# Kernel tuning notes

Measured on AMD Instinct MI355X. Metric: run time of the kernel, lower is better.

## Reference

```python
import jax, jax.numpy as jnp
import numpy as np

N = 100000          # total nodes
E = 1600000         # total edges
B = 500             # graphs in batch
NODES_PER_GRAPH = N // B
D_X, D_XDA = 96, 32
IN = D_X + D_XDA    # 128
HID = 128
OUT = 128


def setup_inputs() -> dict:
    key = jax.random.key(0)
    ks = jax.random.split(key, 12)
    s = 0.05
    x = jax.random.normal(ks[0], (N, D_X), jnp.float32)
    x_da = jax.random.normal(ks[1], (N, D_XDA), jnp.float32)
    edge_index = jax.random.randint(ks[2], (2, E), 0, N, jnp.int32).astype(jnp.int64)
    batch = (jnp.arange(N, dtype=jnp.int64) // NODES_PER_GRAPH)
    rootindex = jnp.arange(B, dtype=jnp.int64) * NODES_PER_GRAPH
    return {
        'x': x, 'x_da': x_da, 'edge_index': edge_index,
        'batch': batch, 'rootindex': rootindex,
        'td_w1': jax.random.normal(ks[3], (IN, HID), jnp.float32) * s,
        'td_b1': jnp.zeros((HID,), jnp.float32),
        'td_w2': jax.random.normal(ks[4], (HID + IN, OUT), jnp.float32) * s,
        'td_b2': jnp.zeros((OUT,), jnp.float32),
        'bu_w1': jax.random.normal(ks[5], (IN, HID), jnp.float32) * s,
        'bu_b1': jnp.zeros((HID,), jnp.float32),
        'bu_w2': jax.random.normal(ks[6], (HID + IN, OUT), jnp.float32) * s,
        'bu_b2': jnp.zeros((OUT,), jnp.float32),
        'mlp_w1': jax.random.normal(ks[7], ((OUT + HID) * 2, 2 * HID), jnp.float32) * s,
        'mlp_b1': jnp.zeros((2 * HID,), jnp.float32),
        'mlp_w2': jax.random.normal(ks[8], (2 * HID, 2), jnp.float32) * s,
        'mlp_b2': jnp.zeros((2,), jnp.float32),
    }


def gcn_conv(h, src, dst, W, b):
    # PyG GCNConv: h' = D^{-1/2} (A + I) D^{-1/2} (h W) + b,
    # messages flow src -> dst, deg counts incoming edges + self loop.
    h = h @ W                                              # [N, out]
    deg = jax.ops.segment_sum(jnp.ones((src.shape[0],), h.dtype), dst,
                              num_segments=N) + 1.0        # self loop
    dinv = jax.lax.rsqrt(deg)                              # deg >= 1
    norm = dinv[src] * dinv[dst]                           # [E]
    agg = jax.ops.segment_sum(h[src] * norm[:, None], dst, num_segments=N)
    agg = agg + h * (dinv * dinv)[:, None]                 # self-loop term
    return agg + b


def branch(x0, src, dst, w1, b1, w2, b2, batch, rootindex):
    # x0: [N, IN] = cat(x, x_da)
    x1 = x0
    h = gcn_conv(x0, src, dst, w1, b1)                     # [N, HID]
    x2 = h
    root1 = x1[rootindex[batch]]                           # root-extend gather
    h = jax.nn.relu(jnp.concatenate([h, root1], axis=1))   # dropout off (eval)
    h = jax.nn.relu(gcn_conv(h, src, dst, w2, b2))         # [N, OUT]
    root2 = x2[rootindex[batch]]
    h = jnp.concatenate([h, root2], axis=1)                # [N, OUT+HID]
    # scatter_mean over graphs
    sums = jax.ops.segment_sum(h, batch, num_segments=B)
    cnt = jax.ops.segment_sum(jnp.ones((N,), h.dtype), batch, num_segments=B)
    return sums / cnt[:, None]                             # [B, OUT+HID]


def reference(x, x_da, edge_index, batch, rootindex,
              td_w1, td_b1, td_w2, td_b2,
              bu_w1, bu_b1, bu_w2, bu_b2,
              mlp_w1, mlp_b1, mlp_w2, mlp_b2):
    x0 = jnp.concatenate([x, x_da], axis=1)                # [N, IN]
    src, dst = edge_index[0], edge_index[1]
    td = branch(x0, src, dst, td_w1, td_b1, td_w2, td_b2, batch, rootindex)
    bu = branch(x0, dst, src, bu_w1, bu_b1, bu_w2, bu_b2, batch, rootindex)
    g = jnp.concatenate([bu, td], axis=1)                  # [B, 4*HID]
    h = jax.nn.relu(g @ mlp_w1 + mlp_b1)
    return h @ mlp_w2 + mlp_b2                             # [B, 2]
```

## Files before the change

### kernel.cpp

```cpp
#include <hip/hip_runtime.h>

#define NN 100000
#define NE 1600000
#define NB 500
#define NPG 200
#define BS 128
#define NBUK 782
#define SLAB 2560
#define EPB3 2048
#define NEB3 782
#define NBLK 1563

typedef unsigned short ushortT;
typedef __attribute__((ext_vector_type(8))) short bf16x8;
typedef __attribute__((ext_vector_type(4))) float f32x4;

#define MFMA16(a, b, c) __builtin_amdgcn_mfma_f32_16x16x32_bf16(a, b, c, 0, 0, 0)

__device__ inline ushortT f2bf(float f) {
    unsigned u = __float_as_uint(f);
    return (ushortT)((u + 0x7FFF + ((u >> 16) & 1)) >> 16);
}
__device__ inline float bf2f(ushortT u) { return __uint_as_float((unsigned)u << 16); }
__device__ inline float4 bf4_to_f4(ushort4 u) {
    return make_float4(bf2f(u.x), bf2f(u.y), bf2f(u.z), bf2f(u.w));
}
__device__ inline bf16x8 cvt8(float4 f0, float4 f1) {
    bf16x8 r;
    r[0] = (short)f2bf(f0.x); r[1] = (short)f2bf(f0.y);
    r[2] = (short)f2bf(f0.z); r[3] = (short)f2bf(f0.w);
    r[4] = (short)f2bf(f1.x); r[5] = (short)f2bf(f1.y);
    r[6] = (short)f2bf(f1.z); r[7] = (short)f2bf(f1.w);
    return r;
}
__device__ inline bf16x8 relu_bf8(uint4 w) {
    bf16x8 r;
    unsigned ws[4] = {w.x, w.y, w.z, w.w};
#pragma unroll
    for (int i = 0; i < 4; i++) {
        unsigned v = ws[i];
        unsigned lo = (v & 0x8000u) ? 0u : (v & 0xFFFFu);
        unsigned hi = (v & 0x80000000u) ? 0u : (v & 0xFFFF0000u);
        r[2 * i]     = (short)lo;
        r[2 * i + 1] = (short)(hi >> 16);
    }
    return r;
}

__global__ void wprep_k(const float* __restrict__ w0, const float* __restrict__ w1,
                        const float* __restrict__ w2, const float* __restrict__ w3,
                        ushortT* __restrict__ wt) {
    int m = blockIdx.x >> 6;
    const float* w = (m == 0) ? w0 : (m == 1) ? w1 : (m == 2) ? w2 : w3;
    ushortT* o = wt + m * 16384;
    int idx = (blockIdx.x & 63) * 256 + threadIdx.x;
    int n = idx >> 7, k = idx & 127;
    o[idx] = f2bf(w[k * 128 + n]);
}

__global__ __launch_bounds__(256) void phase1_k(
    const int* __restrict__ ei,
    int* __restrict__ bcnt_td, int* __restrict__ bcnt_bu,
    int* __restrict__ st_td, int* __restrict__ st_bu,
    const float* __restrict__ x, const float* __restrict__ xda,
    const ushortT* __restrict__ WTa, const ushortT* __restrict__ WTb,
    ushortT* __restrict__ hs_a, ushortT* __restrict__ hs_b) {
    const int t = threadIdx.x;
    if (blockIdx.x < NEB3) {
        __shared__ int h0[NBUK], h1[NBUK];
        for (int i = t; i < NBUK; i += 256) { h0[i] = 0; h1[i] = 0; }
        __syncthreads();
        int base = blockIdx.x * EPB3;
        int a[8], b[8];
#pragma unroll
        for (int j = 0; j < 8; j++) {
            int e = base + t + j * 256;
            a[j] = -1;
            if (e < NE) {
                a[j] = ei[e]; b[j] = ei[NE + e];
                atomicAdd(&h0[b[j] >> 7], 1);
                atomicAdd(&h1[a[j] >> 7], 1);
            }
        }
        __syncthreads();
        for (int i = t; i < NBUK; i += 256) {
            int c0 = h0[i], c1 = h1[i];
            if (c0) h0[i] = atomicAdd(&bcnt_td[i], c0);
            if (c1) h1[i] = atomicAdd(&bcnt_bu[i], c1);
        }
        __syncthreads();
#pragma unroll
        for (int j = 0; j < 8; j++) {
            if (a[j] >= 0) {
                int bk0 = b[j] >> 7;
                int o0 = atomicAdd(&h0[bk0], 1);
                st_td[bk0 * SLAB + o0] = (a[j] << 7) | (b[j] & 127);
                int bk1 = a[j] >> 7;
                int o1 = atomicAdd(&h1[bk1], 1);
                st_bu[bk1 * SLAB + o1] = (b[j] << 7) | (a[j] & 127);
            }
        }
        return;
    }
    const int blk = blockIdx.x - NEB3;
    const int wv = t >> 6, l = t & 63, lr = l & 15, lk = l >> 4;
    const int row0 = blk * 64;
    const int cb0 = (wv * 2) * 16, cb1 = (wv * 2 + 1) * 16;

    bf16x8 bfr[2][2][4];
#pragma unroll
    for (int br = 0; br < 2; br++) {
        const ushortT* WT = br ? WTb : WTa;
#pragma unroll
        for (int c = 0; c < 2; c++) {
            const ushortT* base = WT + (size_t)((wv * 2 + c) * 16 + lr) * 128 + lk * 8;
#pragma unroll
            for (int kk = 0; kk < 4; kk++)
                bfr[br][c][kk] = *reinterpret_cast<const bf16x8*>(base + kk * 32);
        }
    }

#pragma unroll
    for (int rt = 0; rt < 4; rt++) {
        const int rtbase = row0 + rt * 16;
        int arow = rtbase + lr; if (arow >= NN) arow = NN - 1;
        bf16x8 af[4];
#pragma unroll
        for (int kk = 0; kk < 4; kk++) {
            int c8 = kk * 4 + lk;
            float4 f0, f1;
            if (c8 < 12) {
                const float* p = x + (size_t)arow * 96 + c8 * 8;
                f0 = *(const float4*)p; f1 = *(const float4*)(p + 4);
            } else {
                const float* p = xda + (size_t)arow * 32 + (c8 - 12) * 8;
                f0 = *(const float4*)p; f1 = *(const float4*)(p + 4);
            }
            af[kk] = cvt8(f0, f1);
        }
        f32x4 a00 = {0,0,0,0}, a01 = {0,0,0,0}, a10 = {0,0,0,0}, a11 = {0,0,0,0};
#pragma unroll
        for (int kk = 0; kk < 4; kk++) {
            a00 = MFMA16(af[kk], bfr[0][0][kk], a00);
            a01 = MFMA16(af[kk], bfr[0][1][kk], a01);
            a10 = MFMA16(af[kk], bfr[1][0][kk], a10);
            a11 = MFMA16(af[kk], bfr[1][1][kk], a11);
        }
        const int srow = rtbase + lk * 4;
#pragma unroll
        for (int e = 0; e < 4; e++) {
            int r = srow + e;
            if (r < NN) {
                size_t ro = (size_t)r * 128;
                hs_a[ro + cb0 + lr] = f2bf(a00[e]);
                hs_a[ro + cb1 + lr] = f2bf(a01[e]);
                hs_b[ro + cb0 + lr] = f2bf(a10[e]);
                hs_b[ro + cb1 + lr] = f2bf(a11[e]);
            }
        }
    }
}

__global__ __launch_bounds__(256) void place2_k(
    const int* __restrict__ st_td, const int* __restrict__ st_bu,
    const int* __restrict__ bcnt_td, const int* __restrict__ bcnt_bu,
    int* __restrict__ rp_td, int* __restrict__ rp_bu,
    int* __restrict__ csr_td, int* __restrict__ csr_bu,
    float* __restrict__ dinv_td, float* __restrict__ dinv_bu) {
    const int dir = blockIdx.x >= NBUK;
    const int bucket = dir ? blockIdx.x - NBUK : blockIdx.x;
    const int* stage = (dir ? st_bu : st_td) + bucket * SLAB;
    const int* bcnt = dir ? bcnt_bu : bcnt_td;
    const int n = bcnt[bucket];
    int* rp = dir ? rp_bu : rp_td;
    int* csr = dir ? csr_bu : csr_td;
    float* dinv = dir ? dinv_bu : dinv_td;
    const int t = threadIdx.x;

    __shared__ int rw[4];
    __shared__ int sh_obase;
    int part = 0;
    for (int i = t; i < bucket; i += 256) part += bcnt[i];
#pragma unroll
    for (int off = 32; off; off >>= 1) part += __shfl_down(part, off);
    if ((t & 63) == 0) rw[t >> 6] = part;
    __syncthreads();
    if (t == 0) sh_obase = rw[0] + rw[1] + rw[2] + rw[3];
    __syncthreads();
    const int obase = sh_obase;

    const int node0 = bucket << 7;
    __shared__ int lcnt[BS], lsc[BS], lcur[BS];
    if (t < BS) lcnt[t] = 0;
    __syncthreads();
    for (int i = t; i < n; i += 256) atomicAdd(&lcnt[stage[i] & 127], 1);
    __syncthreads();
    if (t < BS) lsc[t] = lcnt[t];
    __syncthreads();
#pragma unroll
    for (int off = 1; off < BS; off <<= 1) {
        int add = (t < BS && t >= off) ? lsc[t - off] : 0;
        __syncthreads();
        if (t < BS) lsc[t] += add;
        __syncthreads();
    }
    if (t < BS) {
        int excl = lsc[t] - lcnt[t];
        lcur[t] = obase + excl;
        int node = node0 + t;
        if (node < NN) {
            rp[node] = obase + excl;
            dinv[node] = rsqrtf((float)(lcnt[t] + 1));
        }
    }
    if (bucket == NBUK - 1 && t == 0) rp[NN] = obase + n;
    __syncthreads();
    for (int i = t; i < n; i += 256) {
        int s = stage[i];
        int off = atomicAdd(&lcur[s & 127], 1);
        csr[off] = (int)((unsigned)s >> 7);
    }
}

__global__ __launch_bounds__(256) void gemm2x_k(
    const ushortT* __restrict__ agg_a, const ushortT* __restrict__ agg_b,
    const ushortT* __restrict__ WTa, const ushortT* __restrict__ WTb,
    const float* __restrict__ rm_a, const float* __restrict__ rm_b,
    ushortT* __restrict__ hs_a, ushortT* __restrict__ hs_b) {
    const int brn = blockIdx.x >= NBLK;
    const ushortT* agg = brn ? agg_b : agg_a;
    const ushortT* WT  = brn ? WTb : WTa;
    const float* rm    = brn ? rm_b : rm_a;
    ushortT* hs        = brn ? hs_b : hs_a;
    const int blk = brn ? blockIdx.x - NBLK : blockIdx.x;
    const int t = threadIdx.x;
    const int wv = t >> 6, l = t & 63, lr = l & 15, lk = l >> 4;
    const int row0 = blk * 64;
    const int cb0 = (wv * 2) * 16, cb1 = (wv * 2 + 1) * 16;

    bf16x8 bfr[2][4];
#pragma unroll
    for (int c = 0; c < 2; c++) {
        const ushortT* base = WT + (size_t)((wv * 2 + c) * 16 + lr) * 128 + lk * 8;
#pragma unroll
        for (int kk = 0; kk < 4; kk++)
            bfr[c][kk] = *reinterpret_cast<const bf16x8*>(base + kk * 32);
    }

#pragma unroll
    for (int rt = 0; rt < 4; rt++) {
        const int rtbase = row0 + rt * 16;
        int arow = rtbase + lr; if (arow >= NN) arow = NN - 1;
        const ushortT* ap = agg + (size_t)arow * 128 + lk * 8;
        bf16x8 af[4];
#pragma unroll
        for (int kk = 0; kk < 4; kk++)
            af[kk] = relu_bf8(*reinterpret_cast<const uint4*>(ap + kk * 32));
        f32x4 a0 = {0,0,0,0}, a1 = {0,0,0,0};
#pragma unroll
        for (int kk = 0; kk < 4; kk++) {
            a0 = MFMA16(af[kk], bfr[0][kk], a0);
            a1 = MFMA16(af[kk], bfr[1][kk], a1);
        }
        const int srow = rtbase + lk * 4;
#pragma unroll
        for (int e = 0; e < 4; e++) {
            int r = srow + e;
            if (r < NN) {
                int bg = r / NPG;
                size_t ro = (size_t)r * 128;
                float r0 = rm[(size_t)bg * 128 + cb0 + lr];
                float r1 = rm[(size_t)bg * 128 + cb1 + lr];
                hs[ro + cb0 + lr] = f2bf(a0[e] + r0);
                hs[ro + cb1 + lr] = f2bf(a1[e] + r1);
            }
        }
    }
}

template <int MODE>
__global__ __launch_bounds__(256) void gather32_k(
    const int* __restrict__ rp_a, const int* __restrict__ csr_a,
    const float* __restrict__ dinv_a, const ushortT* __restrict__ hs_a,
    const float* __restrict__ bias_a,
    const int* __restrict__ rp_b, const int* __restrict__ csr_b,
    const float* __restrict__ dinv_b, const ushortT* __restrict__ hs_b,
    const float* __restrict__ bias_b,
    ushortT* __restrict__ out_a, ushortT* __restrict__ out_b,
    float* __restrict__ gbuf) {
    const int t = threadIdx.x;
    const int v = blockIdx.x * 8 + (t >> 5);
    const int lane = t & 31;
    __shared__ float sacc[256];
    if (MODE == 1) { sacc[t] = 0.f; __syncthreads(); }

    int ba = rp_a[v], ea = rp_a[v + 1];
    int bb = rp_b[v], eb = rp_b[v + 1];
    float dva = dinv_a[v], dvb = dinv_b[v];
    float4 fs = bf4_to_f4(((const ushort4*)(hs_a + (size_t)v * 128))[lane]);
    float4 acc_a = make_float4(fs.x * dva, fs.y * dva, fs.z * dva, fs.w * dva);
    fs = bf4_to_f4(((const ushort4*)(hs_b + (size_t)v * 128))[lane]);
    float4 acc_b = make_float4(fs.x * dvb, fs.y * dvb, fs.z * dvb, fs.w * dvb);

    while (ba < ea || bb < eb) {
        int na = ea - ba; if (na > 32) na = 32; if (na < 0) na = 0;
        int nb = eb - bb; if (nb > 32) nb = 32; if (nb < 0) nb = 0;
        int ia = (lane < na) ? csr_a[ba + lane] : 0;
        int ib = (lane < nb) ? csr_b[bb + lane] : 0;
        float fa = dinv_a[ia];
        float fb = dinv_b[ib];
        for (int i = 0; i < 32; i += 8) {
            if (i >= na && i >= nb) break;
            ushort4 ua[8], ub[8];
            float da8[8], db8[8];
            if (i < na) {
#pragma unroll
                for (int j = 0; j < 8; j++) {
                    int s = __shfl(ia, i + j, 32);
                    da8[j] = __shfl(fa, i + j, 32);
                    ua[j] = ((const ushort4*)(hs_a + (size_t)s * 128))[lane];
                }
            }
            if (i < nb) {
#pragma unroll
                for (int j = 0; j < 8; j++) {
                    int s = __shfl(ib, i + j, 32);
                    db8[j] = __shfl(fb, i + j, 32);
                    ub[j] = ((const ushort4*)(hs_b + (size_t)s * 128))[lane];
                }
            }
            if (i < na) {
#pragma unroll
                for (int j = 0; j < 8; j++)
                    if (i + j < na) {
                        float4 f = bf4_to_f4(ua[j]);
                        acc_a.x = fmaf(f.x, da8[j], acc_a.x);
                        acc_a.y = fmaf(f.y, da8[j], acc_a.y);
                        acc_a.z = fmaf(f.z, da8[j], acc_a.z);
                        acc_a.w = fmaf(f.w, da8[j], acc_a.w);
                    }
            }
            if (i < nb) {
#pragma unroll
                for (int j = 0; j < 8; j++)
                    if (i + j < nb) {
                        float4 f = bf4_to_f4(ub[j]);
                        acc_b.x = fmaf(f.x, db8[j], acc_b.x);
                        acc_b.y = fmaf(f.y, db8[j], acc_b.y);
                        acc_b.z = fmaf(f.z, db8[j], acc_b.z);
                        acc_b.w = fmaf(f.w, db8[j], acc_b.w);
                    }
            }
        }
        ba += 32; bb += 32;
    }

    float4 pa = ((const float4*)bias_a)[lane];
    float4 pb = ((const float4*)bias_b)[lane];
    float4 oa = make_float4(fmaf(acc_a.x, dva, pa.x), fmaf(acc_a.y, dva, pa.y),
                            fmaf(acc_a.z, dva, pa.z), fmaf(acc_a.w, dva, pa.w));
    float4 ob = make_float4(fmaf(acc_b.x, dvb, pb.x), fmaf(acc_b.y, dvb, pb.y),
                            fmaf(acc_b.z, dvb, pb.z), fmaf(acc_b.w, dvb, pb.w));
    if (MODE == 0) {
        ((ushort4*)(out_a + (size_t)v * 128))[lane] =
            make_ushort4(f2bf(oa.x), f2bf(oa.y), f2bf(oa.z), f2bf(oa.w));
        ((ushort4*)(out_b + (size_t)v * 128))[lane] =
            make_ushort4(f2bf(ob.x), f2bf(ob.y), f2bf(ob.z), f2bf(ob.w));
    } else {
        const float sc = 1.0f / NPG;
        oa.x = fmaxf(oa.x, 0.f) * sc; oa.y = fmaxf(oa.y, 0.f) * sc;
        oa.z = fmaxf(oa.z, 0.f) * sc; oa.w = fmaxf(oa.w, 0.f) * sc;
        ob.x = fmaxf(ob.x, 0.f) * sc; ob.y = fmaxf(ob.y, 0.f) * sc;
        ob.z = fmaxf(ob.z, 0.f) * sc; ob.w = fmaxf(ob.w, 0.f) * sc;
        atomicAdd(&sacc[lane * 4 + 0], oa.x);
        atomicAdd(&sacc[lane * 4 + 1], oa.y);
        atomicAdd(&sacc[lane * 4 + 2], oa.z);
        atomicAdd(&sacc[lane * 4 + 3], oa.w);
        atomicAdd(&sacc[128 + lane * 4 + 0], ob.x);
        atomicAdd(&sacc[128 + lane * 4 + 1], ob.y);
        atomicAdd(&sacc[128 + lane * 4 + 2], ob.z);
        atomicAdd(&sacc[128 + lane * 4 + 3], ob.w);
        __syncthreads();
        int g = (blockIdx.x * 8) / NPG;
        unsafeAtomicAdd(&gbuf[(size_t)g * 256 + t], sacc[t]);
    }
}

__global__ void roots_k(
    const float* __restrict__ x, const float* __restrict__ xda,
    const int* __restrict__ root,
    const ushortT* __restrict__ agg_a, const ushortT* __restrict__ agg_b,
    const float* __restrict__ W2a, const float* __restrict__ W2b,
    float* __restrict__ x2a, float* __restrict__ x2b,
    float* __restrict__ rma, float* __restrict__ rmb) {
    __shared__ float xr[128];
    int b = blockIdx.x, t = threadIdx.x;
    int r = root[b];
    if (t < 128) {
        float val = (t < 96) ? x[(size_t)r * 96 + t] : xda[(size_t)r * 32 + (t - 96)];
        xr[t] = fmaxf(val, 0.f);
    }
    __syncthreads();
    int br = t >> 7, c = t & 127;
    const ushortT* agg = br ? agg_b : agg_a;
    const float* W2 = br ? W2b : W2a;
    float* x2 = br ? x2b : x2a;
    float* rm = br ? rmb : rma;
    x2[(size_t)b * 128 + c] = bf2f(agg[(size_t)r * 128 + c]);
    float acc = 0.f;
#pragma unroll 8
    for (int k = 0; k < 128; k++)
        acc = fmaf(xr[k], W2[(size_t)(128 + k) * 128 + c], acc);
    rm[(size_t)b * 128 + c] = acc;
}

__global__ void mlp_k(const float* __restrict__ gbuf,
                      const float* __restrict__ x2a, const float* __restrict__ x2b,
                      const float* __restrict__ w1, const float* __restrict__ b1,
                      const float* __restrict__ w2, const float* __restrict__ b2,
                      float* __restrict__ out) {
    __shared__ float gs[512];
    __shared__ float parts[4][2];
    int b = blockIdx.x, t = threadIdx.x;
    gs[t]       = (t < 128) ? gbuf[(size_t)b * 256 + t]
                            : x2a[(size_t)b * 128 + (t - 128)];
    gs[256 + t] = (t < 128) ? gbuf[(size_t)b * 256 + 128 + t]
                            : x2b[(size_t)b * 128 + (t - 128)];
    __syncthreads();
    float acc = b1[t];
#pragma unroll 8
    for (int k = 0; k < 512; k++)
        acc = fmaf(gs[k], w1[(size_t)k * 256 + t], acc);
    float hv = fmaxf(acc, 0.f);
    float p0 = hv * w2[t * 2 + 0];
    float p1 = hv * w2[t * 2 + 1];
#pragma unroll
    for (int off = 32; off; off >>= 1) {
        p0 += __shfl_down(p0, off);
        p1 += __shfl_down(p1, off);
    }
    int w = t >> 6;
    if ((t & 63) == 0) { parts[w][0] = p0; parts[w][1] = p1; }
    __syncthreads();
    if (t == 0) {
        out[b * 2 + 0] = parts[0][0] + parts[1][0] + parts[2][0] + parts[3][0] + b2[0];
        out[b * 2 + 1] = parts[0][1] + parts[1][1] + parts[2][1] + parts[3][1] + b2[1];
    }
}

extern "C" void kernel_launch(void* const* d_in, const int* in_sizes, int n_in,
                              void* d_out, int out_size, void* d_ws, size_t ws_size,
                              hipStream_t stream) {
    const float* x     = (const float*)d_in[0];
    const float* xda   = (const float*)d_in[1];
    const int*   ei    = (const int*)d_in[2];
    const int*   root  = (const int*)d_in[4];
    const float* td_w1 = (const float*)d_in[5];
    const float* td_b1 = (const float*)d_in[6];
    const float* td_w2 = (const float*)d_in[7];
    const float* td_b2 = (const float*)d_in[8];
    const float* bu_w1 = (const float*)d_in[9];
    const float* bu_b1 = (const float*)d_in[10];
    const float* bu_w2 = (const float*)d_in[11];
    const float* bu_b2 = (const float*)d_in[12];
    const float* mw1   = (const float*)d_in[13];
    const float* mb1   = (const float*)d_in[14];
    const float* mw2   = (const float*)d_in[15];
    const float* mb2   = (const float*)d_in[16];
    float* out = (float*)d_out;

    ushortT* agg_bu  = (ushortT*)d_ws;
    ushortT* agg_td  = agg_bu + (size_t)NN * 128;
    ushortT* hs_bu   = agg_td + (size_t)NN * 128;
    ushortT* hs_td   = hs_bu + (size_t)NN * 128;
    float*   dinv_td = (float*)(hs_td + (size_t)NN * 128);
    float*   dinv_bu = dinv_td + NN;
    float*   x2_bu   = dinv_bu + NN;
    float*   x2_td   = x2_bu + (size_t)NB * 128;
    float*   rm_bu   = x2_td + (size_t)NB * 128;
    float*   rm_td   = rm_bu + (size_t)NB * 128;
    float*   gbuf    = rm_td + (size_t)NB * 128;
    ushortT* wt1_bu  = (ushortT*)(gbuf + (size_t)NB * 256);
    ushortT* wt1_td  = wt1_bu + 16384;
    ushortT* wt2_bu  = wt1_td + 16384;
    ushortT* wt2_td  = wt2_bu + 16384;
    int*     bcnt_td = (int*)(wt2_td + 16384);
    int*     bcnt_bu = bcnt_td + NBUK;
    int*     rp_td   = bcnt_bu + NBUK;
    int*     rp_bu   = rp_td + NN + 1;
    int*     csr_td  = rp_bu + NN + 1;
    int*     csr_bu  = csr_td + NE;
    int*     st_td   = (int*)agg_bu;
    int*     st_bu   = st_td + NBUK * SLAB;

    hipMemsetAsync(bcnt_td, 0, (size_t)(2 * NBUK) * sizeof(int), stream);
    hipMemsetAsync(gbuf, 0, (size_t)NB * 256 * sizeof(float), stream);

    wprep_k<<<4 * 64, 256, 0, stream>>>(bu_w1, td_w1, bu_w2, td_w2, wt1_bu);

    phase1_k<<<NEB3 + NBLK, 256, 0, stream>>>(ei, bcnt_td, bcnt_bu, st_td, st_bu,
                                              x, xda, wt1_bu, wt1_td, hs_bu, hs_td);
    place2_k<<<2 * NBUK, 256, 0, stream>>>(st_td, st_bu, bcnt_td, bcnt_bu,
                                           rp_td, rp_bu, csr_td, csr_bu, dinv_td, dinv_bu);

    gather32_k<0><<<NN / 8, 256, 0, stream>>>(
        rp_bu, csr_bu, dinv_bu, hs_bu, bu_b1,
        rp_td, csr_td, dinv_td, hs_td, td_b1, agg_bu, agg_td, nullptr);

    roots_k<<<NB, 256, 0, stream>>>(x, xda, root, agg_bu, agg_td, bu_w2, td_w2,
                                    x2_bu, x2_td, rm_bu, rm_td);

    gemm2x_k<<<2 * NBLK, 256, 0, stream>>>(agg_bu, agg_td, wt2_bu, wt2_td,
                                           rm_bu, rm_td, hs_bu, hs_td);

    gather32_k<1><<<NN / 8, 256, 0, stream>>>(
        rp_bu, csr_bu, dinv_bu, hs_bu, bu_b2,
        rp_td, csr_td, dinv_td, hs_td, td_b2, nullptr, nullptr, gbuf);

    mlp_k<<<NB, 256, 0, stream>>>(gbuf, x2_bu, x2_td, mw1, mb1, mw2, mb2, out);
}
```

Baseline: 542.0 us.

## Prescale node features by dinv to drop per-edge normalization in gathers

Folds the source-side D^{-1/2} factor into the stored feature rows. The first layer's rows are rescaled in place inside the CSR placement kernel, and the second layer's rows are scaled in the GEMM epilogue. The gather kernels then sum neighbour rows with plain adds and apply the destination dinv once at the end. This removes the per-edge dinv loads and shuffles, at the cost of an extra read-modify-write pass over the first-layer features and an extra bf16 rounding of the scaled values.

After: 541.5 us. No clear change (-0.1%).

```diff
diff --git a/kernel.cpp b/kernel.cpp
--- a/kernel.cpp
+++ b/kernel.cpp
@@ -24,6 +24,11 @@
 __device__ inline float bf2f(ushortT u) { return __uint_as_float((unsigned)u << 16); }
 __device__ inline float4 bf4_to_f4(ushort4 u) {
     return make_float4(bf2f(u.x), bf2f(u.y), bf2f(u.z), bf2f(u.w));
+}
+__device__ inline unsigned scale2bf(unsigned w, float dv) {
+    float lo = __uint_as_float(w << 16) * dv;
+    float hi = __uint_as_float(w & 0xFFFF0000u) * dv;
+    return (unsigned)f2bf(lo) | ((unsigned)f2bf(hi) << 16);
 }
 __device__ inline bf16x8 cvt8(float4 f0, float4 f1) {
     bf16x8 r;
@@ -166,7 +171,8 @@
     const int* __restrict__ bcnt_td, const int* __restrict__ bcnt_bu,
     int* __restrict__ rp_td, int* __restrict__ rp_bu,
     int* __restrict__ csr_td, int* __restrict__ csr_bu,
-    float* __restrict__ dinv_td, float* __restrict__ dinv_bu) {
+    float* __restrict__ dinv_td, float* __restrict__ dinv_bu,
+    ushortT* __restrict__ hs_td, ushortT* __restrict__ hs_bu) {
     const int dir = blockIdx.x >= NBUK;
     const int bucket = dir ? blockIdx.x - NBUK : blockIdx.x;
     const int* stage = (dir ? st_bu : st_td) + bucket * SLAB;
@@ -175,6 +181,7 @@
     int* rp = dir ? rp_bu : rp_td;
     int* csr = dir ? csr_bu : csr_td;
     float* dinv = dir ? dinv_bu : dinv_td;
+    ushortT* hs = dir ? hs_bu : hs_td;
     const int t = threadIdx.x;
 
     __shared__ int rw[4];
@@ -191,6 +198,7 @@
 
     const int node0 = bucket << 7;
     __shared__ int lcnt[BS], lsc[BS], lcur[BS];
+    __shared__ float sdinv[BS];
     if (t < BS) lcnt[t] = 0;
     __syncthreads();
     for (int i = t; i < n; i += 256) atomicAdd(&lcnt[stage[i] & 127], 1);
@@ -207,10 +215,12 @@
     if (t < BS) {
         int excl = lsc[t] - lcnt[t];
         lcur[t] = obase + excl;
+        float dv = rsqrtf((float)(lcnt[t] + 1));
+        sdinv[t] = dv;
         int node = node0 + t;
         if (node < NN) {
             rp[node] = obase + excl;
-            dinv[node] = rsqrtf((float)(lcnt[t] + 1));
+            dinv[node] = dv;
         }
     }
     if (bucket == NBUK - 1 && t == 0) rp[NN] = obase + n;
@@ -220,17 +230,29 @@
         int off = atomicAdd(&lcur[s & 127], 1);
         csr[off] = (int)((unsigned)s >> 7);
     }
+
+    int nvalid = NN - node0; if (nvalid > BS) nvalid = BS;
+    uint4* hrow = (uint4*)(hs + (size_t)node0 * 128);
+    for (int i = t; i < nvalid * 16; i += 256) {
+        float dv = sdinv[i >> 4];
+        uint4 w = hrow[i];
+        w.x = scale2bf(w.x, dv); w.y = scale2bf(w.y, dv);
+        w.z = scale2bf(w.z, dv); w.w = scale2bf(w.w, dv);
+        hrow[i] = w;
+    }
 }
 
 __global__ __launch_bounds__(256) void gemm2x_k(
     const ushortT* __restrict__ agg_a, const ushortT* __restrict__ agg_b,
     const ushortT* __restrict__ WTa, const ushortT* __restrict__ WTb,
     const float* __restrict__ rm_a, const float* __restrict__ rm_b,
+    const float* __restrict__ dinv_a, const float* __restrict__ dinv_b,
     ushortT* __restrict__ hs_a, ushortT* __restrict__ hs_b) {
     const int brn = blockIdx.x >= NBLK;
     const ushortT* agg = brn ? agg_b : agg_a;
     const ushortT* WT  = brn ? WTb : WTa;
     const float* rm    = brn ? rm_b : rm_a;
+    const float* dinv  = brn ? dinv_b : dinv_a;
     ushortT* hs        = brn ? hs_b : hs_a;
     const int blk = brn ? blockIdx.x - NBLK : blockIdx.x;
     const int t = threadIdx.x;
@@ -263,6 +285,8 @@
             a1 = MFMA16(af[kk], bfr[1][kk], a1);
         }
         const int srow = rtbase + lk * 4;
+        float4 dv = *(const float4*)(dinv + srow);
+        const float* dvp = (const float*)&dv;
 #pragma unroll
         for (int e = 0; e < 4; e++) {
             int r = srow + e;
@@ -271,8 +295,8 @@
                 size_t ro = (size_t)r * 128;
                 float r0 = rm[(size_t)bg * 128 + cb0 + lr];
                 float r1 = rm[(size_t)bg * 128 + cb1 + lr];
-                hs[ro + cb0 + lr] = f2bf(a0[e] + r0);
-                hs[ro + cb1 + lr] = f2bf(a1[e] + r1);
+                hs[ro + cb0 + lr] = f2bf((a0[e] + r0) * dvp[e]);
+                hs[ro + cb1 + lr] = f2bf((a1[e] + r1) * dvp[e]);
             }
         }
     }
@@ -296,28 +320,21 @@
 
     int ba = rp_a[v], ea = rp_a[v + 1];
     int bb = rp_b[v], eb = rp_b[v + 1];
-    float dva = dinv_a[v], dvb = dinv_b[v];
-    float4 fs = bf4_to_f4(((const ushort4*)(hs_a + (size_t)v * 128))[lane]);
-    float4 acc_a = make_float4(fs.x * dva, fs.y * dva, fs.z * dva, fs.w * dva);
-    fs = bf4_to_f4(((const ushort4*)(hs_b + (size_t)v * 128))[lane]);
-    float4 acc_b = make_float4(fs.x * dvb, fs.y * dvb, fs.z * dvb, fs.w * dvb);
+    float4 acc_a = bf4_to_f4(((const ushort4*)(hs_a + (size_t)v * 128))[lane]);
+    float4 acc_b = bf4_to_f4(((const ushort4*)(hs_b + (size_t)v * 128))[lane]);
 
     while (ba < ea || bb < eb) {
         int na = ea - ba; if (na > 32) na = 32; if (na < 0) na = 0;
         int nb = eb - bb; if (nb > 32) nb = 32; if (nb < 0) nb = 0;
         int ia = (lane < na) ? csr_a[ba + lane] : 0;
         int ib = (lane < nb) ? csr_b[bb + lane] : 0;
-        float fa = dinv_a[ia];
-        float fb = dinv_b[ib];
         for (int i = 0; i < 32; i += 8) {
             if (i >= na && i >= nb) break;
             ushort4 ua[8], ub[8];
-            float da8[8], db8[8];
             if (i < na) {
 #pragma unroll
                 for (int j = 0; j < 8; j++) {
                     int s = __shfl(ia, i + j, 32);
-                    da8[j] = __shfl(fa, i + j, 32);
                     ua[j] = ((const ushort4*)(hs_a + (size_t)s * 128))[lane];
                 }
             }
@@ -325,7 +342,6 @@
 #pragma unroll
                 for (int j = 0; j < 8; j++) {
                     int s = __shfl(ib, i + j, 32);
-                    db8[j] = __shfl(fb, i + j, 32);
                     ub[j] = ((const ushort4*)(hs_b + (size_t)s * 128))[lane];
                 }
             }
@@ -334,10 +350,7 @@
                 for (int j = 0; j < 8; j++)
                     if (i + j < na) {
                         float4 f = bf4_to_f4(ua[j]);
-                        acc_a.x = fmaf(f.x, da8[j], acc_a.x);
-                        acc_a.y = fmaf(f.y, da8[j], acc_a.y);
-                        acc_a.z = fmaf(f.z, da8[j], acc_a.z);
-                        acc_a.w = fmaf(f.w, da8[j], acc_a.w);
+                        acc_a.x += f.x; acc_a.y += f.y; acc_a.z += f.z; acc_a.w += f.w;
                     }
             }
             if (i < nb) {
@@ -345,22 +358,20 @@
                 for (int j = 0; j < 8; j++)
                     if (i + j < nb) {
                         float4 f = bf4_to_f4(ub[j]);
-                        acc_b.x = fmaf(f.x, db8[j], acc_b.x);
-                        acc_b.y = fmaf(f.y, db8[j], acc_b.y);
-                        acc_b.z = fmaf(f.z, db8[j], acc_b.z);
-                        acc_b.w = fmaf(f.w, db8[j], acc_b.w);
+                        acc_b.x += f.x; acc_b.y += f.y; acc_b.z += f.z; acc_b.w += f.w;
                     }
             }
         }
         ba += 32; bb += 32;
     }
 
+    float da = dinv_a[v], db = dinv_b[v];
     float4 pa = ((const float4*)bias_a)[lane];
     float4 pb = ((const float4*)bias_b)[lane];
-    float4 oa = make_float4(fmaf(acc_a.x, dva, pa.x), fmaf(acc_a.y, dva, pa.y),
-                            fmaf(acc_a.z, dva, pa.z), fmaf(acc_a.w, dva, pa.w));
-    float4 ob = make_float4(fmaf(acc_b.x, dvb, pb.x), fmaf(acc_b.y, dvb, pb.y),
-                            fmaf(acc_b.z, dvb, pb.z), fmaf(acc_b.w, dvb, pb.w));
+    float4 oa = make_float4(fmaf(acc_a.x, da, pa.x), fmaf(acc_a.y, da, pa.y),
+                            fmaf(acc_a.z, da, pa.z), fmaf(acc_a.w, da, pa.w));
+    float4 ob = make_float4(fmaf(acc_b.x, db, pb.x), fmaf(acc_b.y, db, pb.y),
+                            fmaf(acc_b.z, db, pb.z), fmaf(acc_b.w, db, pb.w));
     if (MODE == 0) {
         ((ushort4*)(out_a + (size_t)v * 128))[lane] =
             make_ushort4(f2bf(oa.x), f2bf(oa.y), f2bf(oa.z), f2bf(oa.w));
@@ -501,7 +512,8 @@
     phase1_k<<<NEB3 + NBLK, 256, 0, stream>>>(ei, bcnt_td, bcnt_bu, st_td, st_bu,
                                               x, xda, wt1_bu, wt1_td, hs_bu, hs_td);
     place2_k<<<2 * NBUK, 256, 0, stream>>>(st_td, st_bu, bcnt_td, bcnt_bu,
-                                           rp_td, rp_bu, csr_td, csr_bu, dinv_td, dinv_bu);
+                                           rp_td, rp_bu, csr_td, csr_bu,
+                                           dinv_td, dinv_bu, hs_td, hs_bu);
 
     gather32_k<0><<<NN / 8, 256, 0, stream>>>(
         rp_bu, csr_bu, dinv_bu, hs_bu, bu_b1,
@@ -511,7 +523,7 @@
                                     x2_bu, x2_td, rm_bu, rm_td);
 
     gemm2x_k<<<2 * NBLK, 256, 0, stream>>>(agg_bu, agg_td, wt2_bu, wt2_td,
-                                           rm_bu, rm_td, hs_bu, hs_td);
+                                           rm_bu, rm_td, dinv_bu, dinv_td, hs_bu, hs_td);
 
     gather32_k<1><<<NN / 8, 256, 0, stream>>>(
         rp_bu, csr_bu, dinv_bu, hs_bu, bu_b2,
```

## Widen CSR buckets, fold root kernels into phase1/gemm, replace atomic mean with gmean

Applied to the files above, without the earlier changes.

Bucket size for the edge sort grows from 128 to 256 nodes, halving the bucket count and doubling edges per histogram block. The root-matmul work moves into extra blocks of phase1 and the root x2 copy into extra blocks of gemm2x, so roots_k and its launch disappear. The two memsets are replaced by zeroing bcnt inside wprep_k, and gbuf no longer needs clearing. The second gather now writes relu'd bf16 node features instead of doing shared and global atomics for the graph mean, and a new gmean_k reduces 200 rows per graph, trading atomics for an extra write plus reread of the node features.

Result: faster. 451.7 us (-16.7%).

```diff
diff --git a/kernel.cpp b/kernel.cpp
--- a/kernel.cpp
+++ b/kernel.cpp
@@ -4,11 +4,11 @@
 #define NE 1600000
 #define NB 500
 #define NPG 200
-#define BS 128
-#define NBUK 782
-#define SLAB 2560
-#define EPB3 2048
-#define NEB3 782
+#define BS 256
+#define NBUK 391
+#define SLAB 4608
+#define EPB4 4096
+#define NEB4 391
 #define NBLK 1563
 
 typedef unsigned short ushortT;
@@ -49,7 +49,10 @@
 
 __global__ void wprep_k(const float* __restrict__ w0, const float* __restrict__ w1,
                         const float* __restrict__ w2, const float* __restrict__ w3,
-                        ushortT* __restrict__ wt) {
+                        ushortT* __restrict__ wt, int* __restrict__ bcnt) {
+    if (blockIdx.x == 0) {
+        for (int i = threadIdx.x; i < 2 * NBUK; i += 256) bcnt[i] = 0;
+    }
     int m = blockIdx.x >> 6;
     const float* w = (m == 0) ? w0 : (m == 1) ? w1 : (m == 2) ? w2 : w3;
     ushortT* o = wt + m * 16384;
@@ -64,22 +67,25 @@
     int* __restrict__ st_td, int* __restrict__ st_bu,
     const float* __restrict__ x, const float* __restrict__ xda,
     const ushortT* __restrict__ WTa, const ushortT* __restrict__ WTb,
-    ushortT* __restrict__ hs_a, ushortT* __restrict__ hs_b) {
+    ushortT* __restrict__ hs_a, ushortT* __restrict__ hs_b,
+    const int* __restrict__ root,
+    const float* __restrict__ W2a, const float* __restrict__ W2b,
+    float* __restrict__ rm_a, float* __restrict__ rm_b) {
     const int t = threadIdx.x;
-    if (blockIdx.x < NEB3) {
+    if (blockIdx.x < NEB4) {
         __shared__ int h0[NBUK], h1[NBUK];
         for (int i = t; i < NBUK; i += 256) { h0[i] = 0; h1[i] = 0; }
         __syncthreads();
-        int base = blockIdx.x * EPB3;
-        int a[8], b[8];
-#pragma unroll
-        for (int j = 0; j < 8; j++) {
+        int base = blockIdx.x * EPB4;
+        int a[16], b[16];
+#pragma unroll
+        for (int j = 0; j < 16; j++) {
             int e = base + t + j * 256;
             a[j] = -1;
             if (e < NE) {
                 a[j] = ei[e]; b[j] = ei[NE + e];
-                atomicAdd(&h0[b[j] >> 7], 1);
-                atomicAdd(&h1[a[j] >> 7], 1);
+                atomicAdd(&h0[b[j] >> 8], 1);
+                atomicAdd(&h1[a[j] >> 8], 1);
             }
         }
         __syncthreads();
@@ -90,19 +96,38 @@
         }
         __syncthreads();
 #pragma unroll
-        for (int j = 0; j < 8; j++) {
+        for (int j = 0; j < 16; j++) {
             if (a[j] >= 0) {
-                int bk0 = b[j] >> 7;
+                int bk0 = b[j] >> 8;
                 int o0 = atomicAdd(&h0[bk0], 1);
-                st_td[bk0 * SLAB + o0] = (a[j] << 7) | (b[j] & 127);
-                int bk1 = a[j] >> 7;
+                st_td[bk0 * SLAB + o0] = (a[j] << 8) | (b[j] & 255);
+                int bk1 = a[j] >> 8;
                 int o1 = atomicAdd(&h1[bk1], 1);
-                st_bu[bk1 * SLAB + o1] = (b[j] << 7) | (a[j] & 127);
+                st_bu[bk1 * SLAB + o1] = (b[j] << 8) | (a[j] & 255);
             }
         }
         return;
     }
-    const int blk = blockIdx.x - NEB3;
+    if (blockIdx.x >= NEB4 + NBLK) {
+        int b = blockIdx.x - NEB4 - NBLK;
+        __shared__ float xr[128];
+        int r = root[b];
+        if (t < 128) {
+            float val = (t < 96) ? x[(size_t)r * 96 + t] : xda[(size_t)r * 32 + (t - 96)];
+            xr[t] = fmaxf(val, 0.f);
+        }
+        __syncthreads();
+        int br = t >> 7, c = t & 127;
+        const float* W2 = br ? W2b : W2a;
+        float* rm = br ? rm_b : rm_a;
+        float acc = 0.f;
+#pragma unroll 8
+        for (int k = 0; k < 128; k++)
+            acc = fmaf(xr[k], W2[(size_t)(128 + k) * 128 + c], acc);
+        rm[(size_t)b * 128 + c] = acc;
+        return;
+    }
+    const int blk = blockIdx.x - NEB4;
     const int wv = t >> 6, l = t & 63, lr = l & 15, lk = l >> 4;
     const int row0 = blk * 64;
     const int cb0 = (wv * 2) * 16, cb1 = (wv * 2 + 1) * 16;
@@ -189,22 +214,22 @@
     __syncthreads();
     const int obase = sh_obase;
 
-    const int node0 = bucket << 7;
+    const int node0 = bucket << 8;
     __shared__ int lcnt[BS], lsc[BS], lcur[BS];
-    if (t < BS) lcnt[t] = 0;
-    __syncthreads();
-    for (int i = t; i < n; i += 256) atomicAdd(&lcnt[stage[i] & 127], 1);
-    __syncthreads();
-    if (t < BS) lsc[t] = lcnt[t];
+    lcnt[t] = 0;
+    __syncthreads();
+    for (int i = t; i < n; i += 256) atomicAdd(&lcnt[stage[i] & 255], 1);
+    __syncthreads();
+    lsc[t] = lcnt[t];
     __syncthreads();
 #pragma unroll
     for (int off = 1; off < BS; off <<= 1) {
-        int add = (t < BS && t >= off) ? lsc[t - off] : 0;
+        int add = (t >= off) ? lsc[t - off] : 0;
         __syncthreads();
-        if (t < BS) lsc[t] += add;
+        lsc[t] += add;
         __syncthreads();
     }
-    if (t < BS) {
+    {
         int excl = lsc[t] - lcnt[t];
         lcur[t] = obase + excl;
         int node = node0 + t;
@@ -217,8 +242,8 @@
     __syncthreads();
     for (int i = t; i < n; i += 256) {
         int s = stage[i];
-        int off = atomicAdd(&lcur[s & 127], 1);
-        csr[off] = (int)((unsigned)s >> 7);
+        int off = atomicAdd(&lcur[s & 255], 1);
+        csr[off] = (int)((unsigned)s >> 8);
     }
 }
 
@@ -226,14 +251,24 @@
     const ushortT* __restrict__ agg_a, const ushortT* __restrict__ agg_b,
     const ushortT* __restrict__ WTa, const ushortT* __restrict__ WTb,
     const float* __restrict__ rm_a, const float* __restrict__ rm_b,
+    const int* __restrict__ root, float* __restrict__ x2a, float* __restrict__ x2b,
     ushortT* __restrict__ hs_a, ushortT* __restrict__ hs_b) {
+    const int t = threadIdx.x;
+    if (blockIdx.x >= 2 * NBLK) {
+        int b = blockIdx.x - 2 * NBLK;
+        int br = t >> 7, c = t & 127;
+        const ushortT* agg = br ? agg_b : agg_a;
+        float* x2 = br ? x2b : x2a;
+        int r = root[b];
+        x2[(size_t)b * 128 + c] = bf2f(agg[(size_t)r * 128 + c]);
+        return;
+    }
     const int brn = blockIdx.x >= NBLK;
     const ushortT* agg = brn ? agg_b : agg_a;
     const ushortT* WT  = brn ? WTb : WTa;
     const float* rm    = brn ? rm_b : rm_a;
     ushortT* hs        = brn ? hs_b : hs_a;
     const int blk = brn ? blockIdx.x - NBLK : blockIdx.x;
-    const int t = threadIdx.x;
     const int wv = t >> 6, l = t & 63, lr = l & 15, lk = l >> 4;
     const int row0 = blk * 64;
     const int cb0 = (wv * 2) * 16, cb1 = (wv * 2 + 1) * 16;
@@ -279,21 +314,17 @@
 }
 
 template <int MODE>
-__global__ __launch_bounds__(256) void gather32_k(
+__global__ __launch_bounds__(256) void gather2x_k(
     const int* __restrict__ rp_a, const int* __restrict__ csr_a,
     const float* __restrict__ dinv_a, const ushortT* __restrict__ hs_a,
     const float* __restrict__ bias_a,
     const int* __restrict__ rp_b, const int* __restrict__ csr_b,
     const float* __restrict__ dinv_b, const ushortT* __restrict__ hs_b,
     const float* __restrict__ bias_b,
-    ushortT* __restrict__ out_a, ushortT* __restrict__ out_b,
-    float* __restrict__ gbuf) {
-    const int t = threadIdx.x;
-    const int v = blockIdx.x * 8 + (t >> 5);
-    const int lane = t & 31;
-    __shared__ float sacc[256];
-    if (MODE == 1) { sacc[t] = 0.f; __syncthreads(); }
-
+    ushortT* __restrict__ out_a, ushortT* __restrict__ out_b) {
+    int v = blockIdx.x * 8 + (threadIdx.x >> 5);
+    if (v >= NN) return;
+    const int lane = threadIdx.x & 31;
     int ba = rp_a[v], ea = rp_a[v + 1];
     int bb = rp_b[v], eb = rp_b[v + 1];
     float dva = dinv_a[v], dvb = dinv_b[v];
@@ -361,57 +392,27 @@
                             fmaf(acc_a.z, dva, pa.z), fmaf(acc_a.w, dva, pa.w));
     float4 ob = make_float4(fmaf(acc_b.x, dvb, pb.x), fmaf(acc_b.y, dvb, pb.y),
                             fmaf(acc_b.z, dvb, pb.z), fmaf(acc_b.w, dvb, pb.w));
-    if (MODE == 0) {
-        ((ushort4*)(out_a + (size_t)v * 128))[lane] =
-            make_ushort4(f2bf(oa.x), f2bf(oa.y), f2bf(oa.z), f2bf(oa.w));
-        ((ushort4*)(out_b + (size_t)v * 128))[lane] =
-            make_ushort4(f2bf(ob.x), f2bf(ob.y), f2bf(ob.z), f2bf(ob.w));
-    } else {
-        const float sc = 1.0f / NPG;
-        oa.x = fmaxf(oa.x, 0.f) * sc; oa.y = fmaxf(oa.y, 0.f) * sc;
-        oa.z = fmaxf(oa.z, 0.f) * sc; oa.w = fmaxf(oa.w, 0.f) * sc;
-        ob.x = fmaxf(ob.x, 0.f) * sc; ob.y = fmaxf(ob.y, 0.f) * sc;
-        ob.z = fmaxf(ob.z, 0.f) * sc; ob.w = fmaxf(ob.w, 0.f) * sc;
-        atomicAdd(&sacc[lane * 4 + 0], oa.x);
-        atomicAdd(&sacc[lane * 4 + 1], oa.y);
-        atomicAdd(&sacc[lane * 4 + 2], oa.z);
-        atomicAdd(&sacc[lane * 4 + 3], oa.w);
-        atomicAdd(&sacc[128 + lane * 4 + 0], ob.x);
-        atomicAdd(&sacc[128 + lane * 4 + 1], ob.y);
-        atomicAdd(&sacc[128 + lane * 4 + 2], ob.z);
-        atomicAdd(&sacc[128 + lane * 4 + 3], ob.w);
-        __syncthreads();
-        int g = (blockIdx.x * 8) / NPG;
-        unsafeAtomicAdd(&gbuf[(size_t)g * 256 + t], sacc[t]);
-    }
-}
-
-__global__ void roots_k(
-    const float* __restrict__ x, const float* __restrict__ xda,
-    const int* __restrict__ root,
-    const ushortT* __restrict__ agg_a, const ushortT* __restrict__ agg_b,
-    const float* __restrict__ W2a, const float* __restrict__ W2b,
-    float* __restrict__ x2a, float* __restrict__ x2b,
-    float* __restrict__ rma, float* __restrict__ rmb) {
-    __shared__ float xr[128];
+    if (MODE == 1) {
+        oa.x = fmaxf(oa.x, 0.f); oa.y = fmaxf(oa.y, 0.f); oa.z = fmaxf(oa.z, 0.f); oa.w = fmaxf(oa.w, 0.f);
+        ob.x = fmaxf(ob.x, 0.f); ob.y = fmaxf(ob.y, 0.f); ob.z = fmaxf(ob.z, 0.f); ob.w = fmaxf(ob.w, 0.f);
+    }
+    ((ushort4*)(out_a + (size_t)v * 128))[lane] =
+        make_ushort4(f2bf(oa.x), f2bf(oa.y), f2bf(oa.z), f2bf(oa.w));
+    ((ushort4*)(out_b + (size_t)v * 128))[lane] =
+        make_ushort4(f2bf(ob.x), f2bf(ob.y), f2bf(ob.z), f2bf(ob.w));
+}
+
+__global__ void gmean_k(const ushortT* __restrict__ ra, const ushortT* __restrict__ rb,
+                        float* __restrict__ gbuf) {
     int b = blockIdx.x, t = threadIdx.x;
-    int r = root[b];
-    if (t < 128) {
-        float val = (t < 96) ? x[(size_t)r * 96 + t] : xda[(size_t)r * 32 + (t - 96)];
-        xr[t] = fmaxf(val, 0.f);
-    }
-    __syncthreads();
     int br = t >> 7, c = t & 127;
-    const ushortT* agg = br ? agg_b : agg_a;
-    const float* W2 = br ? W2b : W2a;
-    float* x2 = br ? x2b : x2a;
-    float* rm = br ? rmb : rma;
-    x2[(size_t)b * 128 + c] = bf2f(agg[(size_t)r * 128 + c]);
-    float acc = 0.f;
-#pragma unroll 8
-    for (int k = 0; k < 128; k++)
-        acc = fmaf(xr[k], W2[(size_t)(128 + k) * 128 + c], acc);
-    rm[(size_t)b * 128 + c] = acc;
+    const ushortT* src = br ? rb : ra;
+    size_t base = (size_t)b * NPG * 128 + c;
+    float s = 0.f;
+#pragma unroll 4
+    for (int r = 0; r < NPG; r++)
+        s += bf2f(src[base + (size_t)r * 128]);
+    gbuf[(size_t)b * 256 + br * 128 + c] = s * (1.0f / NPG);
 }
 
 __global__ void mlp_k(const float* __restrict__ gbuf,
@@ -493,29 +494,29 @@
     int*     st_td   = (int*)agg_bu;
     int*     st_bu   = st_td + NBUK * SLAB;
 
-    hipMemsetAsync(bcnt_td, 0, (size_t)(2 * NBUK) * sizeof(int), stream);
-    hipMemsetAsync(gbuf, 0, (size_t)NB * 256 * sizeof(float), stream);
-
-    wprep_k<<<4 * 64, 256, 0, stream>>>(bu_w1, td_w1, bu_w2, td_w2, wt1_bu);
-
-    phase1_k<<<NEB3 + NBLK, 256, 0, stream>>>(ei, bcnt_td, bcnt_bu, st_td, st_bu,
-                                              x, xda, wt1_bu, wt1_td, hs_bu, hs_td);
+    wprep_k<<<4 * 64, 256, 0, stream>>>(bu_w1, td_w1, bu_w2, td_w2, wt1_bu, bcnt_td);
+
+    phase1_k<<<NEB4 + NBLK + NB, 256, 0, stream>>>(
+        ei, bcnt_td, bcnt_bu, st_td, st_bu,
+        x, xda, wt1_bu, wt1_td, hs_bu, hs_td,
+        root, bu_w2, td_w2, rm_bu, rm_td);
+
     place2_k<<<2 * NBUK, 256, 0, stream>>>(st_td, st_bu, bcnt_td, bcnt_bu,
-                                           rp_td, rp_bu, csr_td, csr_bu, dinv_td, dinv_bu);
-
-    gather32_k<0><<<NN / 8, 256, 0, stream>>>(
+                                           rp_td, rp_bu, csr_td, csr_bu,
+                                           dinv_td, dinv_bu);
+
+    gather2x_k<0><<<(NN + 7) / 8, 256, 0, stream>>>(
         rp_bu, csr_bu, dinv_bu, hs_bu, bu_b1,
-        rp_td, csr_td, dinv_td, hs_td, td_b1, agg_bu, agg_td, nullptr);
-
-    roots_k<<<NB, 256, 0, stream>>>(x, xda, root, agg_bu, agg_td, bu_w2, td_w2,
-                                    x2_bu, x2_td, rm_bu, rm_td);
-
-    gemm2x_k<<<2 * NBLK, 256, 0, stream>>>(agg_bu, agg_td, wt2_bu, wt2_td,
-                                           rm_bu, rm_td, hs_bu, hs_td);
-
-    gather32_k<1><<<NN / 8, 256, 0, stream>>>(
+        rp_td, csr_td, dinv_td, hs_td, td_b1, agg_bu, agg_td);
+
+    gemm2x_k<<<2 * NBLK + NB, 256, 0, stream>>>(
+        agg_bu, agg_td, wt2_bu, wt2_td, rm_bu, rm_td,
+        root, x2_bu, x2_td, hs_bu, hs_td);
+
+    gather2x_k<1><<<(NN + 7) / 8, 256, 0, stream>>>(
         rp_bu, csr_bu, dinv_bu, hs_bu, bu_b2,
-        rp_td, csr_td, dinv_td, hs_td, td_b2, nullptr, nullptr, gbuf);
-
+        rp_td, csr_td, dinv_td, hs_td, td_b2, agg_bu, agg_td);
+
+    gmean_k<<<NB, 256, 0, stream>>>(agg_bu, agg_td, gbuf);
     mlp_k<<<NB, 256, 0, stream>>>(gbuf, x2_bu, x2_td, mw1, mb1, mw2, mb2, out);
 }
```
